# Kernel tuning notes

Measured on AMD Instinct MI355X. Metric: run time of the kernel, lower is better.

The kernel has to match this reference:

```python
import jax, jax.numpy as jnp
import numpy as np

N_HEADS = 16
HEAD_DIM = 128

def _apply_rope(x, cos, sin):
    # x: [B, H, T, D]; cos/sin: [T, D//2]
    B, H, T, D = x.shape
    xp = x.astype(jnp.float32).reshape(B, H, T, D // 2, 2)
    x0, x1 = xp[..., 0], xp[..., 1]
    c = cos[None, None, :T, :]
    s = sin[None, None, :T, :]
    # complex multiply (x0 + i x1) * (c + i s)
    r0 = x0 * c - x1 * s
    r1 = x0 * s + x1 * c
    out = jnp.stack([r0, r1], axis=-1).reshape(B, H, T, D)
    return out.astype(x.dtype)

def setup_inputs() -> dict:
    key = jax.random.key(0)
    ks = jax.random.split(key, 7)
    B, T, C = 2, 2048, 2048
    Dh = C // N_HEADS
    sc = 1.0 / np.sqrt(C)
    x = jax.random.normal(ks[0], (B, T, C), dtype=jnp.float32)
    # rotary frequencies like precompute_freqs_cis
    pos = jnp.arange(T, dtype=jnp.float32)
    inv = 1.0 / (10000.0 ** (jnp.arange(0, Dh, 2, dtype=jnp.float32) / Dh))
    ang = pos[:, None] * inv[None, :]  # [T, Dh//2]
    freqs_cos = jnp.cos(ang)
    freqs_sin = jnp.sin(ang)
    wq = jax.random.normal(ks[1], (C, C), dtype=jnp.float32) * sc
    wk = jax.random.normal(ks[2], (C, C), dtype=jnp.float32) * sc
    wv = jax.random.normal(ks[3], (C, C), dtype=jnp.float32) * sc
    wo = jax.random.normal(ks[4], (C, C), dtype=jnp.float32) * sc
    return {"x": x, "freqs_cos": freqs_cos, "freqs_sin": freqs_sin,
            "wq": wq, "wk": wk, "wv": wv, "wo": wo}

def reference(x, freqs_cos, freqs_sin, wq, wk, wv, wo):
    B, T, C = x.shape
    H, D = N_HEADS, HEAD_DIM
    # nn.Linear applies x @ W.T
    q = (x @ wq.T).reshape(B, T, H, D).transpose(0, 2, 1, 3)
    k = (x @ wk.T).reshape(B, T, H, D).transpose(0, 2, 1, 3)
    v = (x @ wv.T).reshape(B, T, H, D).transpose(0, 2, 1, 3)
    q = _apply_rope(q, freqs_cos, freqs_sin)
    k = _apply_rope(k, freqs_cos, freqs_sin)
    scale = 1.0 / np.sqrt(D)
    attn = jnp.einsum('bhqd,bhkd->bhqk', q, k) * scale  # [B,H,T,T]
    causal = jnp.tril(jnp.ones((T, T), dtype=bool))
    attn = jnp.where(causal[None, None], attn, -jnp.inf)
    attn = jax.nn.softmax(attn, axis=-1)
    out = jnp.einsum('bhqk,bhkd->bhqd', attn, v)
    out = out.transpose(0, 2, 1, 3).reshape(B, T, C)
    return out @ wo.T
```

## Files before the change

### kernel.cpp

```cpp
#include <hip/hip_runtime.h>
#include <hip/hip_bf16.h>
#include <stdint.h>


typedef short bf16x8 __attribute__((ext_vector_type(8)));
typedef float f32x4  __attribute__((ext_vector_type(4)));

static __device__ __forceinline__ short f2bf(float f) {
  unsigned u = __builtin_bit_cast(unsigned, f);
  u = (u + 0x7fffu + ((u >> 16) & 1u)) >> 16;
  return (short)u;
}
static __device__ __forceinline__ float bf2f(short s) {
  unsigned u = ((unsigned)(unsigned short)s) << 16;
  return __builtin_bit_cast(float, u);
}
static __device__ __forceinline__ void gload_lds16(const void* g, void* l) {
  auto gp = (const __attribute__((address_space(1))) void*)(g);
  auto lp = (__attribute__((address_space(3))) void*)(l);
  __builtin_amdgcn_global_load_lds(gp, lp, 16, 0, 0);
}
#define VMCNT(n) asm volatile("s_waitcnt vmcnt(" #n ")" ::: "memory")

__global__ __launch_bounds__(256) void cast8_kernel(const float* __restrict__ in,
                                                    short* __restrict__ out, int n8) {
  int g = blockIdx.x * 256 + threadIdx.x;
  if (g >= n8) return;
  const float4* p = (const float4*)(in + (size_t)g * 8);
  float4 a = p[0], b = p[1];
  bf16x8 o;
  o[0] = f2bf(a.x); o[1] = f2bf(a.y); o[2] = f2bf(a.z); o[3] = f2bf(a.w);
  o[4] = f2bf(b.x); o[5] = f2bf(b.y); o[6] = f2bf(b.z); o[7] = f2bf(b.w);
  *(bf16x8*)(out + (size_t)g * 8) = o;
}

__global__ __launch_bounds__(256) void castw_kernel(const float* __restrict__ w0,
                                                    const float* __restrict__ w1,
                                                    const float* __restrict__ w2,
                                                    const float* __restrict__ w3,
                                                    short* __restrict__ out) {
  int seg = blockIdx.y;
  const float* in = (seg == 0) ? w0 : (seg == 1) ? w1 : (seg == 2) ? w2 : w3;
  short* o = out + (size_t)seg * 4194304;
  int g = blockIdx.x * 256 + threadIdx.x;
  const float4* p = (const float4*)(in + (size_t)g * 8);
  float4 a = p[0], b = p[1];
  bf16x8 v;
  v[0] = f2bf(a.x); v[1] = f2bf(a.y); v[2] = f2bf(a.z); v[3] = f2bf(a.w);
  v[4] = f2bf(b.x); v[5] = f2bf(b.y); v[6] = f2bf(b.z); v[7] = f2bf(b.w);
  *(bf16x8*)(o + (size_t)g * 8) = v;
}

__global__ __launch_bounds__(256) void transpose_v(const short* __restrict__ vb,
                                                   short* __restrict__ vt) {
  __shared__ char L[8192] __attribute__((aligned(128)));
  int bx = blockIdx.x;
  int bh = bx >> 6, rest = bx & 63, tt = rest >> 1, td = rest & 1;
  int t0 = tt * 64, d0 = td * 64;
  size_t base = (size_t)bh * (2048 * 128);
#pragma unroll
  for (int it = 0; it < 2; ++it) {
    int c = it * 256 + threadIdx.x;
    int t = c >> 3, dc = c & 7;
    bf16x8 v = *(const bf16x8*)(vb + base + (size_t)(t0 + t) * 128 + d0 + dc * 8);
#pragma unroll
    for (int i = 0; i < 8; ++i) {
      int d = dc * 8 + i;
      int g = (d & 7) ^ ((d >> 3) & 7);
      *(short*)(L + d * 128 + (((t >> 3) ^ g) * 16) + (t & 7) * 2) = v[i];
    }
  }
  __syncthreads();
#pragma unroll
  for (int it = 0; it < 2; ++it) {
    int c = it * 256 + threadIdx.x;
    int dr = c >> 3, tc = c & 7;
    int g = (dr & 7) ^ ((dr >> 3) & 7);
    bf16x8 v = *(const bf16x8*)(L + dr * 128 + ((tc ^ g) * 16));
    *(bf16x8*)(vt + base + (size_t)(d0 + dr) * 2048 + t0 + tc * 8) = v;
  }
}

template <int MODE>
__global__ __launch_bounds__(512, 1) void gemm8(const short* __restrict__ A,
                                                const short* __restrict__ W0,
                                                const short* __restrict__ W1,
                                                const short* __restrict__ W2,
                                                short* __restrict__ oq,
                                                short* __restrict__ ok_,
                                                short* __restrict__ ov,
                                                float* __restrict__ of,
                                                const float* __restrict__ fc,
                                                const float* __restrict__ fs,
                                                int NT) {
  const int SB = 49152;
  __shared__ char lds[147456] __attribute__((aligned(128)));
  int nwg = gridDim.x;
  int bid = blockIdx.x;
  int wg = (bid & 7) * (nwg >> 3) + (bid >> 3);
  int mt = wg / NT, nt = wg % NT;
  const int tid = threadIdx.x;
  const int lane = tid & 63;
  const int wid = tid >> 6;
  const int wr = wid >> 2, wc = wid & 3;
  const int l15 = lane & 15, l4 = lane >> 4;
  const short* Wp;
  int n0, wsel = 0;
  if (MODE == 0) {
    wsel = nt >> 3;
    Wp = (wsel == 0) ? W0 : ((wsel == 1) ? W1 : W2);
    n0 = (nt & 7) * 256;
  } else {
    Wp = W0;
    n0 = nt * 256;
  }
  const int m0 = mt * 128;
  const short* Ab = A + (size_t)m0 * 2048;
  const short* Wb = Wp + (size_t)n0 * 2048;

  const f32x4 vzero = {0.f, 0.f, 0.f, 0.f};
  f32x4 acc[4][4];
#pragma unroll
  for (int i = 0; i < 4; ++i)
#pragma unroll
    for (int j = 0; j < 4; ++j) acc[i][j] = vzero;

  auto stage = [&](int b, int t) {
    int k0 = t * 64;
    char* La = lds + b * SB;
    char* Lb = La + 16384;
#pragma unroll
    for (int j = 0; j < 2; ++j) {
      int c = j * 512 + tid;
      int row = c >> 3, slot = c & 7;
      gload_lds16(Ab + (size_t)row * 2048 + k0 + ((slot ^ (row & 7)) * 8),
                  La + (c - lane) * 16);
    }
#pragma unroll
    for (int j = 0; j < 4; ++j) {
      int c = j * 512 + tid;
      int row = c >> 3, slot = c & 7;
      gload_lds16(Wb + (size_t)row * 2048 + k0 + ((slot ^ (row & 7)) * 8),
                  Lb + (c - lane) * 16);
    }
  };

  stage(0, 0);
  stage(1, 1);
  VMCNT(6);
  __builtin_amdgcn_s_barrier();

  int cb = 0, sb = 2;
#pragma unroll 1
  for (int t = 0; t < 32; ++t) {
    if (t + 2 < 32) stage(sb, t + 2);
    const char* La = lds + cb * SB;
    const char* Lb = La + 16384;
#pragma unroll
    for (int kk = 0; kk < 2; ++kk) {
      bf16x8 af[4], wf[4];
#pragma unroll
      for (int i = 0; i < 4; ++i) {
        int Ra = wr * 64 + i * 16 + l15;
        af[i] = *(const bf16x8*)(La + Ra * 128 + (((kk * 4 + l4) ^ (Ra & 7)) << 4));
        int Rb = wc * 64 + i * 16 + l15;
        wf[i] = *(const bf16x8*)(Lb + Rb * 128 + (((kk * 4 + l4) ^ (Rb & 7)) << 4));
      }
      __builtin_amdgcn_s_setprio(1);
#pragma unroll
      for (int mi = 0; mi < 4; ++mi)
#pragma unroll
        for (int ni = 0; ni < 4; ++ni)
          acc[mi][ni] = __builtin_amdgcn_mfma_f32_16x16x32_bf16(af[mi], wf[ni], acc[mi][ni], 0, 0, 0);
      __builtin_amdgcn_s_setprio(0);
    }
    if (t + 2 < 32) { VMCNT(6); } else { VMCNT(0); }
    __builtin_amdgcn_s_barrier();
    cb = (cb == 2) ? 0 : cb + 1;
    sb = (sb == 2) ? 0 : sb + 1;
  }

  if (MODE == 0) {
    short* o = (wsel == 0) ? oq : ((wsel == 1) ? ok_ : ov);
#pragma unroll
    for (int mi = 0; mi < 4; ++mi) {
#pragma unroll
      for (int j = 0; j < 4; ++j) {
        int rr = m0 + wr * 64 + mi * 16 + l4 * 4 + j;
        int b = rr >> 11, t = rr & 2047;
#pragma unroll
        for (int ni = 0; ni < 4; ++ni) {
          int cc = n0 + wc * 64 + ni * 16 + l15;
          int h = cc >> 7, d = cc & 127;
          float v = acc[mi][ni][j];
          if (wsel < 2) {
            float vp = __shfl_xor(v, 1);
            float c = fc[t * 64 + (d >> 1)];
            float s = fs[t * 64 + (d >> 1)];
            v = (lane & 1) ? (vp * s + v * c) : (v * c - vp * s);
            if (wsel == 0) v *= 0.08838834764831845f;
          }
          o[(((size_t)b * 16 + h) * 2048 + t) * 128 + d] = f2bf(v);
        }
      }
    }
  } else {
#pragma unroll
    for (int mi = 0; mi < 4; ++mi)
#pragma unroll
      for (int j = 0; j < 4; ++j) {
        int rr = m0 + wr * 64 + mi * 16 + l4 * 4 + j;
#pragma unroll
        for (int ni = 0; ni < 4; ++ni) {
          int cc = n0 + wc * 64 + ni * 16 + l15;
          of[(size_t)rr * 2048 + cc] = acc[mi][ni][j];
        }
      }
  }
}

__global__ __launch_bounds__(256) void attn_kernel(const short* __restrict__ qb,
                                                   const short* __restrict__ kb,
                                                   const short* __restrict__ vt,
                                                   short* __restrict__ aout) {
  __shared__ char lds[73728] __attribute__((aligned(128)));
  const int tid = threadIdx.x;
  const int lane = tid & 63;
  const int w = tid >> 6;
  const int l15 = lane & 15, l4 = lane >> 4;
  int bid0 = blockIdx.x;
  int bid = (bid0 & 7) * 64 + (bid0 >> 3);
  const int bh = bid >> 4, p = bid & 15;
  const size_t qkbase = (size_t)bh * (2048 * 128);
  char* Pb = lds + 65536 + w * 2048;
  const f32x4 vzero = {0.f, 0.f, 0.f, 0.f};

  auto stage = [&](int b, int kt) {
#pragma unroll
    for (int j = 0; j < 4; ++j) {
      int c = j * 256 + tid;
      int ldsoff = (c - lane) * 16;
      {
        int row = c >> 4, slot = c & 15;
        gload_lds16(kb + qkbase + (size_t)(kt * 64 + row) * 128 + ((slot ^ (row & 7)) * 8),
                    lds + b * 32768 + ldsoff);
      }
      {
        int row = c >> 3, slot = c & 7;
        gload_lds16(vt + qkbase + (size_t)row * 2048 + kt * 64 + ((slot ^ (row & 7)) * 8),
                    lds + b * 32768 + 16384 + ldsoff);
      }
    }
  };

#pragma unroll 1
  for (int half = 0; half < 2; ++half) {
    const int qtile = half ? (31 - p) : p;
    const int qbase = qtile << 6;
    const int qrow = qbase + w * 16 + l15;
    bf16x8 aq[4];
#pragma unroll
    for (int ks = 0; ks < 4; ++ks)
      aq[ks] = *(const bf16x8*)(qb + qkbase + (size_t)qrow * 128 + ks * 32 + l4 * 8);
    f32x4 accO[8];
#pragma unroll
    for (int nt = 0; nt < 8; ++nt) accO[nt] = vzero;
    float m_[4], l_[4];
#pragma unroll
    for (int j = 0; j < 4; ++j) { m_[j] = -1e30f; l_[j] = 0.f; }

    stage(0, 0);
    VMCNT(0);
    __builtin_amdgcn_s_barrier();

#pragma unroll 1
    for (int kt = 0; kt <= qtile; ++kt) {
      const int cbuf = kt & 1;
      if (kt < qtile) stage(cbuf ^ 1, kt + 1);
      const char* Kl = lds + cbuf * 32768;
      const char* Vl = Kl + 16384;

      f32x4 s[4];
      __builtin_amdgcn_s_setprio(1);
#pragma unroll
      for (int ct = 0; ct < 4; ++ct) {
        s[ct] = vzero;
        int kcol = ct * 16 + l15;
#pragma unroll
        for (int ks = 0; ks < 4; ++ks) {
          bf16x8 bk = *(const bf16x8*)(Kl + kcol * 256 + ((ks * 64 + l4 * 16) ^ ((kcol & 7) << 4)));
          s[ct] = __builtin_amdgcn_mfma_f32_16x16x32_bf16(aq[ks], bk, s[ct], 0, 0, 0);
        }
      }
      __builtin_amdgcn_s_setprio(0);
      if (kt * 64 + 63 > qbase + w * 16) {
#pragma unroll
        for (int ct = 0; ct < 4; ++ct) {
          int kc = kt * 64 + ct * 16 + l15;
#pragma unroll
          for (int j = 0; j < 4; ++j) {
            int r = qbase + w * 16 + l4 * 4 + j;
            if (kc > r) s[ct][j] = -1e30f;
          }
        }
      }
#pragma unroll
      for (int j = 0; j < 4; ++j) {
        float mx = fmaxf(fmaxf(s[0][j], s[1][j]), fmaxf(s[2][j], s[3][j]));
        mx = fmaxf(mx, __shfl_xor(mx, 1));
        mx = fmaxf(mx, __shfl_xor(mx, 2));
        mx = fmaxf(mx, __shfl_xor(mx, 4));
        mx = fmaxf(mx, __shfl_xor(mx, 8));
        float mn = fmaxf(m_[j], mx);
        float resc = __expf(m_[j] - mn);
        m_[j] = mn;
        float rs = 0.f;
#pragma unroll
        for (int ct = 0; ct < 4; ++ct) {
          float e = __expf(s[ct][j] - mn);
          s[ct][j] = e;
          rs += e;
        }
        rs += __shfl_xor(rs, 1);
        rs += __shfl_xor(rs, 2);
        rs += __shfl_xor(rs, 4);
        rs += __shfl_xor(rs, 8);
        l_[j] = l_[j] * resc + rs;
#pragma unroll
        for (int nt = 0; nt < 8; ++nt) accO[nt][j] *= resc;
      }
#pragma unroll
      for (int ct = 0; ct < 4; ++ct)
#pragma unroll
        for (int j = 0; j < 4; ++j) {
          int r = l4 * 4 + j, cc = ct * 16 + l15;
          *(short*)(Pb + r * 128 + ((cc * 2) ^ ((r & 7) << 4))) = f2bf(s[ct][j]);
        }
      __threadfence_block();
      __builtin_amdgcn_s_setprio(1);
#pragma unroll
      for (int ks2 = 0; ks2 < 2; ++ks2) {
        bf16x8 pa = *(const bf16x8*)(Pb + l15 * 128 + ((ks2 * 64 + l4 * 16) ^ ((l15 & 7) << 4)));
#pragma unroll
        for (int nt = 0; nt < 8; ++nt) {
          int d = nt * 16 + l15;
          bf16x8 bv = *(const bf16x8*)(Vl + d * 128 + ((ks2 * 64 + l4 * 16) ^ ((d & 7) << 4)));
          accO[nt] = __builtin_amdgcn_mfma_f32_16x16x32_bf16(pa, bv, accO[nt], 0, 0, 0);
        }
      }
      __builtin_amdgcn_s_setprio(0);
      VMCNT(0);
      __builtin_amdgcn_s_barrier();
    }
    const int b = bh >> 4, h = bh & 15;
#pragma unroll
    for (int j = 0; j < 4; ++j) {
      float inv = 1.0f / l_[j];
      int t = qbase + w * 16 + l4 * 4 + j;
      size_t obase = ((size_t)(b * 2048 + t)) * 2048 + h * 128;
#pragma unroll
      for (int nt = 0; nt < 8; ++nt)
        aout[obase + nt * 16 + l15] = f2bf(accO[nt][j] * inv);
    }
  }
}

extern "C" void kernel_launch(void* const* d_in, const int* in_sizes, int n_in,
                              void* d_out, int out_size, void* d_ws, size_t ws_size,
                              hipStream_t stream) {
  const float* x  = (const float*)d_in[0];
  const float* fc = (const float*)d_in[1];
  const float* fs = (const float*)d_in[2];
  const float* wq = (const float*)d_in[3];
  const float* wk = (const float*)d_in[4];
  const float* wv = (const float*)d_in[5];
  const float* wo = (const float*)d_in[6];

  short* ws  = (short*)d_ws;
  short* xb  = ws;
  short* wqb = ws + 8388608;
  short* wkb = ws + 12582912;
  short* wvb = ws + 16777216;
  short* wob = ws + 20971520;
  short* qb  = ws + 25165824;
  short* kb  = ws + 33554432;
  short* vb  = ws + 41943040;
  short* vt  = xb;
  short* aout = vb;

  cast8_kernel<<<4096, 256, 0, stream>>>(x, xb, 1048576);
  castw_kernel<<<dim3(2048, 4), 256, 0, stream>>>(wq, wk, wv, wo, wqb);
  gemm8<0><<<768, 512, 0, stream>>>(xb, wqb, wkb, wvb, qb, kb, vb, nullptr, fc, fs, 24);
  transpose_v<<<2048, 256, 0, stream>>>(vb, vt);
  attn_kernel<<<512, 256, 0, stream>>>(qb, kb, vt, aout);
  gemm8<1><<<256, 512, 0, stream>>>(aout, wob, nullptr, nullptr,
                                    nullptr, nullptr, nullptr, (float*)d_out,
                                    nullptr, nullptr, 8);
}
```

Measured before the change: 422.1 us.

## Replace pipelined GEMM with simple 128x128 tile GEMM and rework attention tiling

Drops the triple-buffered, XOR-swizzled 256x128 GEMM in favour of a single-buffered 128x128 tile GEMM with 256 threads and two barriers per 32-wide k step. This doubles the grid for both projections. The attention kernel now uses 512 threads and one 128-row query tile per block, scheduled heaviest-first, instead of pairing two 64-row tiles per block. The GEMM loses load/compute overlap and LDS swizzling, so it risks exposed global latency and bank conflicts in exchange for more blocks and simpler code.

```diff
diff --git a/kernel.cpp b/kernel.cpp
--- a/kernel.cpp
+++ b/kernel.cpp
@@ -82,104 +82,68 @@
 }
 
 template <int MODE>
-__global__ __launch_bounds__(512, 1) void gemm8(const short* __restrict__ A,
-                                                const short* __restrict__ W0,
-                                                const short* __restrict__ W1,
-                                                const short* __restrict__ W2,
-                                                short* __restrict__ oq,
-                                                short* __restrict__ ok_,
-                                                short* __restrict__ ov,
-                                                float* __restrict__ of,
-                                                const float* __restrict__ fc,
-                                                const float* __restrict__ fs,
-                                                int NT) {
-  const int SB = 49152;
-  __shared__ char lds[147456] __attribute__((aligned(128)));
+__global__ __launch_bounds__(256) void gemm_bt(const short* __restrict__ A,
+                                               const short* __restrict__ W0,
+                                               const short* __restrict__ W1,
+                                               const short* __restrict__ W2,
+                                               short* __restrict__ oq,
+                                               short* __restrict__ ok_,
+                                               short* __restrict__ ov,
+                                               float* __restrict__ of,
+                                               const float* __restrict__ fc,
+                                               const float* __restrict__ fs,
+                                               int NT) {
+  __shared__ char lds[16384] __attribute__((aligned(128)));
   int nwg = gridDim.x;
   int bid = blockIdx.x;
   int wg = (bid & 7) * (nwg >> 3) + (bid >> 3);
   int mt = wg / NT, nt = wg % NT;
-  const int tid = threadIdx.x;
-  const int lane = tid & 63;
-  const int wid = tid >> 6;
-  const int wr = wid >> 2, wc = wid & 3;
+  const int lane = threadIdx.x & 63;
+  const int wid = threadIdx.x >> 6;
+  const int wr = wid >> 1, wc = wid & 1;
   const int l15 = lane & 15, l4 = lane >> 4;
   const short* Wp;
   int n0, wsel = 0;
   if (MODE == 0) {
-    wsel = nt >> 3;
+    wsel = nt >> 4;
     Wp = (wsel == 0) ? W0 : ((wsel == 1) ? W1 : W2);
-    n0 = (nt & 7) * 256;
+    n0 = (nt & 15) * 128;
   } else {
     Wp = W0;
-    n0 = nt * 256;
+    n0 = nt * 128;
   }
   const int m0 = mt * 128;
+  const f32x4 vzero = {0.f, 0.f, 0.f, 0.f};
+  f32x4 acc[4][4];
+#pragma unroll
+  for (int i = 0; i < 4; ++i)
+#pragma unroll
+    for (int j = 0; j < 4; ++j) acc[i][j] = vzero;
   const short* Ab = A + (size_t)m0 * 2048;
   const short* Wb = Wp + (size_t)n0 * 2048;
-
-  const f32x4 vzero = {0.f, 0.f, 0.f, 0.f};
-  f32x4 acc[4][4];
-#pragma unroll
-  for (int i = 0; i < 4; ++i)
-#pragma unroll
-    for (int j = 0; j < 4; ++j) acc[i][j] = vzero;
-
-  auto stage = [&](int b, int t) {
-    int k0 = t * 64;
-    char* La = lds + b * SB;
-    char* Lb = La + 16384;
+  for (int k0 = 0; k0 < 2048; k0 += 32) {
 #pragma unroll
     for (int j = 0; j < 2; ++j) {
-      int c = j * 512 + tid;
-      int row = c >> 3, slot = c & 7;
-      gload_lds16(Ab + (size_t)row * 2048 + k0 + ((slot ^ (row & 7)) * 8),
-                  La + (c - lane) * 16);
-    }
-#pragma unroll
-    for (int j = 0; j < 4; ++j) {
-      int c = j * 512 + tid;
-      int row = c >> 3, slot = c & 7;
-      gload_lds16(Wb + (size_t)row * 2048 + k0 + ((slot ^ (row & 7)) * 8),
-                  Lb + (c - lane) * 16);
-    }
-  };
-
-  stage(0, 0);
-  stage(1, 1);
-  VMCNT(6);
-  __builtin_amdgcn_s_barrier();
-
-  int cb = 0, sb = 2;
-#pragma unroll 1
-  for (int t = 0; t < 32; ++t) {
-    if (t + 2 < 32) stage(sb, t + 2);
-    const char* La = lds + cb * SB;
-    const char* Lb = La + 16384;
-#pragma unroll
-    for (int kk = 0; kk < 2; ++kk) {
-      bf16x8 af[4], wf[4];
-#pragma unroll
-      for (int i = 0; i < 4; ++i) {
-        int Ra = wr * 64 + i * 16 + l15;
-        af[i] = *(const bf16x8*)(La + Ra * 128 + (((kk * 4 + l4) ^ (Ra & 7)) << 4));
-        int Rb = wc * 64 + i * 16 + l15;
-        wf[i] = *(const bf16x8*)(Lb + Rb * 128 + (((kk * 4 + l4) ^ (Rb & 7)) << 4));
-      }
-      __builtin_amdgcn_s_setprio(1);
-#pragma unroll
-      for (int mi = 0; mi < 4; ++mi)
-#pragma unroll
-        for (int ni = 0; ni < 4; ++ni)
-          acc[mi][ni] = __builtin_amdgcn_mfma_f32_16x16x32_bf16(af[mi], wf[ni], acc[mi][ni], 0, 0, 0);
-      __builtin_amdgcn_s_setprio(0);
-    }
-    if (t + 2 < 32) { VMCNT(6); } else { VMCNT(0); }
-    __builtin_amdgcn_s_barrier();
-    cb = (cb == 2) ? 0 : cb + 1;
-    sb = (sb == 2) ? 0 : sb + 1;
-  }
-
+      int c = j * 256 + (int)threadIdx.x;
+      int row = c >> 2, slot = c & 3;
+      int ldsoff = (c - lane) * 16;
+      gload_lds16(Ab + (size_t)row * 2048 + k0 + slot * 8, lds + ldsoff);
+      gload_lds16(Wb + (size_t)row * 2048 + k0 + slot * 8, lds + 8192 + ldsoff);
+    }
+    __syncthreads();
+    bf16x8 af[4], wf[4];
+#pragma unroll
+    for (int i = 0; i < 4; ++i) {
+      af[i] = *(const bf16x8*)(lds + (wr * 64 + i * 16 + l15) * 64 + l4 * 16);
+      wf[i] = *(const bf16x8*)(lds + 8192 + (wc * 64 + i * 16 + l15) * 64 + l4 * 16);
+    }
+#pragma unroll
+    for (int i = 0; i < 4; ++i)
+#pragma unroll
+      for (int j = 0; j < 4; ++j)
+        acc[i][j] = __builtin_amdgcn_mfma_f32_16x16x32_bf16(af[i], wf[j], acc[i][j], 0, 0, 0);
+    __syncthreads();
+  }
   if (MODE == 0) {
     short* o = (wsel == 0) ? oq : ((wsel == 1) ? ok_ : ov);
 #pragma unroll
@@ -219,26 +183,29 @@
   }
 }
 
-__global__ __launch_bounds__(256) void attn_kernel(const short* __restrict__ qb,
-                                                   const short* __restrict__ kb,
-                                                   const short* __restrict__ vt,
-                                                   short* __restrict__ aout) {
-  __shared__ char lds[73728] __attribute__((aligned(128)));
+__global__ __launch_bounds__(512, 4) void attn_kernel(const short* __restrict__ qb,
+                                                      const short* __restrict__ kb,
+                                                      const short* __restrict__ vt,
+                                                      short* __restrict__ aout) {
+  __shared__ char lds[81920] __attribute__((aligned(128)));
   const int tid = threadIdx.x;
   const int lane = tid & 63;
   const int w = tid >> 6;
   const int l15 = lane & 15, l4 = lane >> 4;
-  int bid0 = blockIdx.x;
-  int bid = (bid0 & 7) * 64 + (bid0 >> 3);
-  const int bh = bid >> 4, p = bid & 15;
+  const int bid0 = blockIdx.x;
+  const int xcd = bid0 & 7, idx = bid0 >> 3;
+  const int bh = xcd * 4 + (idx & 3);
+  const int qtile = 15 - (idx >> 2);
   const size_t qkbase = (size_t)bh * (2048 * 128);
   char* Pb = lds + 65536 + w * 2048;
   const f32x4 vzero = {0.f, 0.f, 0.f, 0.f};
+  const int qbase = qtile << 7;
+  const int ktmax = 2 * qtile + 1;
 
   auto stage = [&](int b, int kt) {
 #pragma unroll
-    for (int j = 0; j < 4; ++j) {
-      int c = j * 256 + tid;
+    for (int j = 0; j < 2; ++j) {
+      int c = j * 512 + tid;
       int ldsoff = (c - lane) * 16;
       {
         int row = c >> 4, slot = c & 15;
@@ -253,115 +220,110 @@
     }
   };
 
+  const int qrow = qbase + w * 16 + l15;
+  bf16x8 aq[4];
+#pragma unroll
+  for (int ks = 0; ks < 4; ++ks)
+    aq[ks] = *(const bf16x8*)(qb + qkbase + (size_t)qrow * 128 + ks * 32 + l4 * 8);
+  f32x4 accO[8];
+#pragma unroll
+  for (int nt = 0; nt < 8; ++nt) accO[nt] = vzero;
+  float m_[4], l_[4];
+#pragma unroll
+  for (int j = 0; j < 4; ++j) { m_[j] = -1e30f; l_[j] = 0.f; }
+
+  stage(0, 0);
+  VMCNT(0);
+  __builtin_amdgcn_s_barrier();
+
 #pragma unroll 1
-  for (int half = 0; half < 2; ++half) {
-    const int qtile = half ? (31 - p) : p;
-    const int qbase = qtile << 6;
-    const int qrow = qbase + w * 16 + l15;
-    bf16x8 aq[4];
-#pragma unroll
-    for (int ks = 0; ks < 4; ++ks)
-      aq[ks] = *(const bf16x8*)(qb + qkbase + (size_t)qrow * 128 + ks * 32 + l4 * 8);
-    f32x4 accO[8];
-#pragma unroll
-    for (int nt = 0; nt < 8; ++nt) accO[nt] = vzero;
-    float m_[4], l_[4];
-#pragma unroll
-    for (int j = 0; j < 4; ++j) { m_[j] = -1e30f; l_[j] = 0.f; }
-
-    stage(0, 0);
+  for (int kt = 0; kt <= ktmax; ++kt) {
+    const int cbuf = kt & 1;
+    if (kt < ktmax) stage(cbuf ^ 1, kt + 1);
+    const char* Kl = lds + cbuf * 32768;
+    const char* Vl = Kl + 16384;
+
+    f32x4 s[4];
+    __builtin_amdgcn_s_setprio(1);
+#pragma unroll
+    for (int ct = 0; ct < 4; ++ct) {
+      s[ct] = vzero;
+      int kcol = ct * 16 + l15;
+#pragma unroll
+      for (int ks = 0; ks < 4; ++ks) {
+        bf16x8 bk = *(const bf16x8*)(Kl + kcol * 256 + ((ks * 64 + l4 * 16) ^ ((kcol & 7) << 4)));
+        s[ct] = __builtin_amdgcn_mfma_f32_16x16x32_bf16(aq[ks], bk, s[ct], 0, 0, 0);
+      }
+    }
+    __builtin_amdgcn_s_setprio(0);
+    if (kt * 64 + 63 > qbase + w * 16) {
+#pragma unroll
+      for (int ct = 0; ct < 4; ++ct) {
+        int kc = kt * 64 + ct * 16 + l15;
+#pragma unroll
+        for (int j = 0; j < 4; ++j) {
+          int r = qbase + w * 16 + l4 * 4 + j;
+          if (kc > r) s[ct][j] = -1e30f;
+        }
+      }
+    }
+#pragma unroll
+    for (int j = 0; j < 4; ++j) {
+      float mx = fmaxf(fmaxf(s[0][j], s[1][j]), fmaxf(s[2][j], s[3][j]));
+      mx = fmaxf(mx, __shfl_xor(mx, 1));
+      mx = fmaxf(mx, __shfl_xor(mx, 2));
+      mx = fmaxf(mx, __shfl_xor(mx, 4));
+      mx = fmaxf(mx, __shfl_xor(mx, 8));
+      float mn = fmaxf(m_[j], mx);
+      float resc = __expf(m_[j] - mn);
+      m_[j] = mn;
+      float rs = 0.f;
+#pragma unroll
+      for (int ct = 0; ct < 4; ++ct) {
+        float e = __expf(s[ct][j] - mn);
+        s[ct][j] = e;
+        rs += e;
+      }
+      rs += __shfl_xor(rs, 1);
+      rs += __shfl_xor(rs, 2);
+      rs += __shfl_xor(rs, 4);
+      rs += __shfl_xor(rs, 8);
+      l_[j] = l_[j] * resc + rs;
+#pragma unroll
+      for (int nt = 0; nt < 8; ++nt) accO[nt][j] *= resc;
+    }
+#pragma unroll
+    for (int ct = 0; ct < 4; ++ct)
+#pragma unroll
+      for (int j = 0; j < 4; ++j) {
+        int r = l4 * 4 + j, cc = ct * 16 + l15;
+        *(short*)(Pb + r * 128 + ((cc * 2) ^ ((r & 7) << 4))) = f2bf(s[ct][j]);
+      }
+    __threadfence_block();
+    __builtin_amdgcn_s_setprio(1);
+#pragma unroll
+    for (int ks2 = 0; ks2 < 2; ++ks2) {
+      bf16x8 pa = *(const bf16x8*)(Pb + l15 * 128 + ((ks2 * 64 + l4 * 16) ^ ((l15 & 7) << 4)));
+#pragma unroll
+      for (int nt = 0; nt < 8; ++nt) {
+        int d = nt * 16 + l15;
+        bf16x8 bv = *(const bf16x8*)(Vl + d * 128 + ((ks2 * 64 + l4 * 16) ^ ((d & 7) << 4)));
+        accO[nt] = __builtin_amdgcn_mfma_f32_16x16x32_bf16(pa, bv, accO[nt], 0, 0, 0);
+      }
+    }
+    __builtin_amdgcn_s_setprio(0);
     VMCNT(0);
     __builtin_amdgcn_s_barrier();
-
-#pragma unroll 1
-    for (int kt = 0; kt <= qtile; ++kt) {
-      const int cbuf = kt & 1;
-      if (kt < qtile) stage(cbuf ^ 1, kt + 1);
-      const char* Kl = lds + cbuf * 32768;
-      const char* Vl = Kl + 16384;
-
-      f32x4 s[4];
-      __builtin_amdgcn_s_setprio(1);
-#pragma unroll
-      for (int ct = 0; ct < 4; ++ct) {
-        s[ct] = vzero;
-        int kcol = ct * 16 + l15;
-#pragma unroll
-        for (int ks = 0; ks < 4; ++ks) {
-          bf16x8 bk = *(const bf16x8*)(Kl + kcol * 256 + ((ks * 64 + l4 * 16) ^ ((kcol & 7) << 4)));
-          s[ct] = __builtin_amdgcn_mfma_f32_16x16x32_bf16(aq[ks], bk, s[ct], 0, 0, 0);
-        }
-      }
-      __builtin_amdgcn_s_setprio(0);
-      if (kt * 64 + 63 > qbase + w * 16) {
-#pragma unroll
-        for (int ct = 0; ct < 4; ++ct) {
-          int kc = kt * 64 + ct * 16 + l15;
-#pragma unroll
-          for (int j = 0; j < 4; ++j) {
-            int r = qbase + w * 16 + l4 * 4 + j;
-            if (kc > r) s[ct][j] = -1e30f;
-          }
-        }
-      }
-#pragma unroll
-      for (int j = 0; j < 4; ++j) {
-        float mx = fmaxf(fmaxf(s[0][j], s[1][j]), fmaxf(s[2][j], s[3][j]));
-        mx = fmaxf(mx, __shfl_xor(mx, 1));
-        mx = fmaxf(mx, __shfl_xor(mx, 2));
-        mx = fmaxf(mx, __shfl_xor(mx, 4));
-        mx = fmaxf(mx, __shfl_xor(mx, 8));
-        float mn = fmaxf(m_[j], mx);
-        float resc = __expf(m_[j] - mn);
-        m_[j] = mn;
-        float rs = 0.f;
-#pragma unroll
-        for (int ct = 0; ct < 4; ++ct) {
-          float e = __expf(s[ct][j] - mn);
-          s[ct][j] = e;
-          rs += e;
-        }
-        rs += __shfl_xor(rs, 1);
-        rs += __shfl_xor(rs, 2);
-        rs += __shfl_xor(rs, 4);
-        rs += __shfl_xor(rs, 8);
-        l_[j] = l_[j] * resc + rs;
-#pragma unroll
-        for (int nt = 0; nt < 8; ++nt) accO[nt][j] *= resc;
-      }
-#pragma unroll
-      for (int ct = 0; ct < 4; ++ct)
-#pragma unroll
-        for (int j = 0; j < 4; ++j) {
-          int r = l4 * 4 + j, cc = ct * 16 + l15;
-          *(short*)(Pb + r * 128 + ((cc * 2) ^ ((r & 7) << 4))) = f2bf(s[ct][j]);
-        }
-      __threadfence_block();
-      __builtin_amdgcn_s_setprio(1);
-#pragma unroll
-      for (int ks2 = 0; ks2 < 2; ++ks2) {
-        bf16x8 pa = *(const bf16x8*)(Pb + l15 * 128 + ((ks2 * 64 + l4 * 16) ^ ((l15 & 7) << 4)));
-#pragma unroll
-        for (int nt = 0; nt < 8; ++nt) {
-          int d = nt * 16 + l15;
-          bf16x8 bv = *(const bf16x8*)(Vl + d * 128 + ((ks2 * 64 + l4 * 16) ^ ((d & 7) << 4)));
-          accO[nt] = __builtin_amdgcn_mfma_f32_16x16x32_bf16(pa, bv, accO[nt], 0, 0, 0);
-        }
-      }
-      __builtin_amdgcn_s_setprio(0);
-      VMCNT(0);
-      __builtin_amdgcn_s_barrier();
-    }
-    const int b = bh >> 4, h = bh & 15;
-#pragma unroll
-    for (int j = 0; j < 4; ++j) {
-      float inv = 1.0f / l_[j];
-      int t = qbase + w * 16 + l4 * 4 + j;
-      size_t obase = ((size_t)(b * 2048 + t)) * 2048 + h * 128;
-#pragma unroll
-      for (int nt = 0; nt < 8; ++nt)
-        aout[obase + nt * 16 + l15] = f2bf(accO[nt][j] * inv);
-    }
+  }
+  const int b = bh >> 4, h = bh & 15;
+#pragma unroll
+  for (int j = 0; j < 4; ++j) {
+    float inv = 1.0f / l_[j];
+    int t = qbase + w * 16 + l4 * 4 + j;
+    size_t obase = ((size_t)(b * 2048 + t)) * 2048 + h * 128;
+#pragma unroll
+    for (int nt = 0; nt < 8; ++nt)
+      aout[obase + nt * 16 + l15] = f2bf(accO[nt][j] * inv);
   }
 }
 
@@ -390,10 +352,10 @@
 
   cast8_kernel<<<4096, 256, 0, stream>>>(x, xb, 1048576);
   castw_kernel<<<dim3(2048, 4), 256, 0, stream>>>(wq, wk, wv, wo, wqb);
-  gemm8<0><<<768, 512, 0, stream>>>(xb, wqb, wkb, wvb, qb, kb, vb, nullptr, fc, fs, 24);
+  gemm_bt<0><<<1536, 256, 0, stream>>>(xb, wqb, wkb, wvb, qb, kb, vb, nullptr, fc, fs, 48);
   transpose_v<<<2048, 256, 0, stream>>>(vb, vt);
-  attn_kernel<<<512, 256, 0, stream>>>(qb, kb, vt, aout);
-  gemm8<1><<<256, 512, 0, stream>>>(aout, wob, nullptr, nullptr,
-                                    nullptr, nullptr, nullptr, (float*)d_out,
-                                    nullptr, nullptr, 8);
-}
+  attn_kernel<<<512, 512, 0, stream>>>(qb, kb, vt, aout);
+  gemm_bt<1><<<512, 256, 0, stream>>>(aout, wob, nullptr, nullptr,
+                                      nullptr, nullptr, nullptr, (float*)d_out,
+                                      nullptr, nullptr, 16);
+}
```

Result: slower. 491.6 us (+16.5%).
